# Performance work log

Hardware: AMD Instinct MI355X
Metric: run time of the kernel (lower is better)

Reference implementation:

```python
import jax, jax.numpy as jnp
import numpy as np

B, S, IN, OUT = 4, 2048, 4096, 4096


def setup_inputs() -> dict:
    key = jax.random.key(0)
    kx, kw, kb = jax.random.split(key, 3)
    x = jax.random.randint(kx, (B, S, IN), -127, 128, dtype=jnp.int8)
    weight = jax.random.randint(kw, (OUT, IN), -127, 128, dtype=jnp.int8)
    # original module initializes bias to zeros(int32); use random int32 to exercise the add
    bias = jax.random.randint(kb, (1, OUT), -1000, 1000, dtype=jnp.int32)
    return {"x": x, "weight": weight, "bias": bias}


def reference(x, weight, bias):
    x_shape = x.shape
    x2 = x.reshape(-1, x_shape[-1])  # [tokens, IN], int8
    # dot_general with preferred_element_type=int32 -> int8 inputs, int32 accumulate
    y = jax.lax.dot_general(
        x2, weight,
        dimension_numbers=(((1,), (1,)), ((), ())),
        preferred_element_type=jnp.int32,
    )  # [tokens, OUT] int32
    y = y + bias  # broadcast [1, OUT] int32
    return y.reshape(*x_shape[:-1], -1)
```

## Files before the change

### kernel.cpp

```cpp
#include <hip/hip_runtime.h>
#include <stdint.h>

#define M_TOT 8192
#define N_TOT 4096
#define K_TOT 4096

typedef int v4i  __attribute__((ext_vector_type(4)));
typedef int v16i __attribute__((ext_vector_type(16)));

__device__ __forceinline__ void gload_lds16(const void* g, void* l) {
    __builtin_amdgcn_global_load_lds(
        (const __attribute__((address_space(1))) unsigned int*)g,
        (__attribute__((address_space(3))) unsigned int*)l,
        16, 0, 0);
}

#define WAIT_VMCNT0() __builtin_amdgcn_s_waitcnt(0x0f70)
#define WAIT_VMCNT8() __builtin_amdgcn_s_waitcnt(0x0f78)

__global__ __launch_bounds__(256) void pack_i32_to_i8(
        const int4* __restrict__ src, int* __restrict__ dst, int n4) {
    int idx = blockIdx.x * 1024 + threadIdx.x;
#pragma unroll
    for (int u = 0; u < 4; ++u, idx += 256) {
        const int4 a = src[idx];
        dst[idx] = (a.x & 255) | ((a.y & 255) << 8) |
                   ((a.z & 255) << 16) | (a.w << 24);
    }
}

__global__ __launch_bounds__(256, 1) void i8gemm_bias(
        const signed char* __restrict__ x,
        const signed char* __restrict__ w,
        const int* __restrict__ bias,
        int* __restrict__ out) {
    __shared__ __align__(16) signed char la[3][256 * 64];
    __shared__ __align__(16) signed char lb[3][256 * 64];

    const int tid  = threadIdx.x;
    const int lane = tid & 63;
    const int wv   = tid >> 6;
    const int l31  = lane & 31;
    const int kh   = lane >> 5;
    const int wr   = wv >> 1;
    const int wc   = wv & 1;

    const int flat = blockIdx.y * gridDim.x + blockIdx.x;
    const int swz  = (flat & 7) * 64 + (flat >> 3);
    const int bn0  = (swz & 15) * 256;
    const int bm0  = (swz >> 4) * 256;

    int bv[4];
#pragma unroll
    for (int j = 0; j < 4; ++j) bv[j] = bias[bn0 + wc * 128 + j * 32 + l31];
    v16i acc[4][4];
#pragma unroll
    for (int i = 0; i < 4; ++i)
#pragma unroll
        for (int j = 0; j < 4; ++j)
#pragma unroll
            for (int r = 0; r < 16; ++r) acc[i][j][r] = bv[j];

    const int fc = (lane & 3) ^ ((lane >> 3) & 3);
    const signed char* pa = x + (long)(bm0 + wv * 64 + (lane >> 2)) * K_TOT + fc * 16;
    const signed char* pb = w + (long)(bn0 + wv * 64 + (lane >> 2)) * K_TOT + fc * 16;
    const int lbase = wv * 64 * 64;

    const int swr = (l31 >> 1) & 3;

    signed char* A0 = &la[0][0]; signed char* A1 = &la[1][0]; signed char* A2 = &la[2][0];
    signed char* B0 = &lb[0][0]; signed char* B1 = &lb[1][0]; signed char* B2 = &lb[2][0];

#pragma unroll
    for (int i = 0; i < 4; ++i) {
        gload_lds16(pa + (long)i * 16 * K_TOT, A0 + lbase + i * 1024);
        gload_lds16(pb + (long)i * 16 * K_TOT, B0 + lbase + i * 1024);
    }
#pragma unroll
    for (int i = 0; i < 4; ++i) {
        gload_lds16(pa + 64 + (long)i * 16 * K_TOT, A1 + lbase + i * 1024);
        gload_lds16(pb + 64 + (long)i * 16 * K_TOT, B1 + lbase + i * 1024);
    }

    const int NT = K_TOT / 64;
    for (int kt = 0; kt < NT; ++kt) {
        if (kt == NT - 1) { WAIT_VMCNT0(); } else { WAIT_VMCNT8(); }
        __builtin_amdgcn_s_barrier();
        __builtin_amdgcn_sched_barrier(0);

        if (kt + 2 < NT) {
            const long k0 = (long)(kt + 2) * 64;
#pragma unroll
            for (int i = 0; i < 4; ++i) {
                gload_lds16(pa + k0 + (long)i * 16 * K_TOT, A2 + lbase + i * 1024);
                gload_lds16(pb + k0 + (long)i * 16 * K_TOT, B2 + lbase + i * 1024);
            }
        }
        __builtin_amdgcn_sched_barrier(0);

        v4i af[2][4], bf[2][4];
#pragma unroll
        for (int kk = 0; kk < 2; ++kk) {
            const int cs = ((kk * 2 + kh) ^ swr) * 16;
#pragma unroll
            for (int i = 0; i < 4; ++i) {
                af[kk][i] = *(const v4i*)(A0 + (wr * 128 + i * 32 + l31) * 64 + cs);
                bf[kk][i] = *(const v4i*)(B0 + (wc * 128 + i * 32 + l31) * 64 + cs);
            }
        }
        __builtin_amdgcn_sched_barrier(0);

#pragma unroll
        for (int kk = 0; kk < 2; ++kk)
#pragma unroll
            for (int i = 0; i < 4; ++i)
#pragma unroll
                for (int j = 0; j < 4; ++j)
                    acc[i][j] = __builtin_amdgcn_mfma_i32_32x32x32_i8(
                        af[kk][i], bf[kk][j], acc[i][j], 0, 0, 0);

        signed char* t;
        t = A0; A0 = A1; A1 = A2; A2 = t;
        t = B0; B0 = B1; B1 = B2; B2 = t;
    }

#pragma unroll
    for (int i = 0; i < 4; ++i) {
        const int mbase = bm0 + wr * 128 + i * 32 + 4 * kh;
#pragma unroll
        for (int j = 0; j < 4; ++j) {
            const int n = bn0 + wc * 128 + j * 32 + l31;
#pragma unroll
            for (int r = 0; r < 16; ++r) {
                const int m = mbase + (r & 3) + 8 * (r >> 2);
                out[(long)m * N_TOT + n] = acc[i][j][r];
            }
        }
    }
}

extern "C" void kernel_launch(void* const* d_in, const int* in_sizes, int n_in,
                              void* d_out, int out_size, void* d_ws, size_t ws_size,
                              hipStream_t stream) {
    const int* x32  = (const int*)d_in[0];
    const int* w32  = (const int*)d_in[1];
    const int* bias = (const int*)d_in[2];
    int*       out  = (int*)d_out;

    signed char* xp = (signed char*)d_ws;
    signed char* wp = (signed char*)d_ws + (size_t)M_TOT * K_TOT;

    const int n4x = (M_TOT * K_TOT) / 4;
    const int n4w = (N_TOT * K_TOT) / 4;
    pack_i32_to_i8<<<n4x / 1024, 256, 0, stream>>>((const int4*)x32, (int*)xp, n4x);
    pack_i32_to_i8<<<n4w / 1024, 256, 0, stream>>>((const int4*)w32, (int*)wp, n4w);

    dim3 grid(N_TOT / 256, M_TOT / 256);
    i8gemm_bias<<<grid, 256, 0, stream>>>(xp, wp, bias, out);
}
```

Before: 404.6 us.

## Software-pipeline LDS fragment reads against MFMA across k-halves

Splits each 64-wide k tile into two halves with separate register fragment sets. The first half of the next tile is read from LDS during the current tile's second-half MFMAs, with the wait and barrier moved mid-iteration. This is meant to hide LDS read latency behind matrix-core work instead of stalling before each tile's MFMAs. It needs more registers, and the waitcnt and barrier placement now also waits on LDS counters, which risks correctness if it is wrong.

```diff
diff --git a/kernel.cpp b/kernel.cpp
--- a/kernel.cpp
+++ b/kernel.cpp
@@ -15,8 +15,11 @@
         16, 0, 0);
 }
 
-#define WAIT_VMCNT0() __builtin_amdgcn_s_waitcnt(0x0f70)
-#define WAIT_VMCNT8() __builtin_amdgcn_s_waitcnt(0x0f78)
+#define WAIT_V8_L0() __builtin_amdgcn_s_waitcnt(0x0078)
+#define WAIT_V0_L0() __builtin_amdgcn_s_waitcnt(0x0070)
+#define WAIT_V8()    __builtin_amdgcn_s_waitcnt(0x0f78)
+#define SBAR()       __builtin_amdgcn_s_barrier()
+#define SFENCE()     __builtin_amdgcn_sched_barrier(0)
 
 __global__ __launch_bounds__(256) void pack_i32_to_i8(
         const int4* __restrict__ src, int* __restrict__ dst, int n4) {
@@ -66,7 +69,11 @@
     const signed char* pb = w + (long)(bn0 + wv * 64 + (lane >> 2)) * K_TOT + fc * 16;
     const int lbase = wv * 64 * 64;
 
-    const int swr = (l31 >> 1) & 3;
+    const int swr  = (l31 >> 1) & 3;
+    const int aoff = (wr * 128 + l31) * 64;
+    const int boff = (wc * 128 + l31) * 64;
+    const int cs0  = ((kh    ) ^ swr) * 16;
+    const int cs1  = ((2 + kh) ^ swr) * 16;
 
     signed char* A0 = &la[0][0]; signed char* A1 = &la[1][0]; signed char* A2 = &la[2][0];
     signed char* B0 = &lb[0][0]; signed char* B1 = &lb[1][0]; signed char* B2 = &lb[2][0];
@@ -81,13 +88,26 @@
         gload_lds16(pa + 64 + (long)i * 16 * K_TOT, A1 + lbase + i * 1024);
         gload_lds16(pb + 64 + (long)i * 16 * K_TOT, B1 + lbase + i * 1024);
     }
+    WAIT_V8();
+    SBAR();
+    SFENCE();
+
+    v4i a0[4], b0[4], a1[4], b1[4];
+#pragma unroll
+    for (int i = 0; i < 4; ++i) {
+        a0[i] = *(const v4i*)(A0 + aoff + i * 2048 + cs0);
+        b0[i] = *(const v4i*)(B0 + boff + i * 2048 + cs0);
+    }
 
     const int NT = K_TOT / 64;
     for (int kt = 0; kt < NT; ++kt) {
-        if (kt == NT - 1) { WAIT_VMCNT0(); } else { WAIT_VMCNT8(); }
-        __builtin_amdgcn_s_barrier();
-        __builtin_amdgcn_sched_barrier(0);
-
+        SFENCE();
+#pragma unroll
+        for (int i = 0; i < 4; ++i) {
+            a1[i] = *(const v4i*)(A0 + aoff + i * 2048 + cs1);
+            b1[i] = *(const v4i*)(B0 + boff + i * 2048 + cs1);
+        }
+        SFENCE();
         if (kt + 2 < NT) {
             const long k0 = (long)(kt + 2) * 64;
 #pragma unroll
@@ -96,28 +116,32 @@
                 gload_lds16(pb + k0 + (long)i * 16 * K_TOT, B2 + lbase + i * 1024);
             }
         }
-        __builtin_amdgcn_sched_barrier(0);
-
-        v4i af[2][4], bf[2][4];
+        SFENCE();
 #pragma unroll
-        for (int kk = 0; kk < 2; ++kk) {
-            const int cs = ((kk * 2 + kh) ^ swr) * 16;
+        for (int i = 0; i < 4; ++i)
+#pragma unroll
+            for (int j = 0; j < 4; ++j)
+                acc[i][j] = __builtin_amdgcn_mfma_i32_32x32x32_i8(
+                    a0[i], b0[j], acc[i][j], 0, 0, 0);
+        SFENCE();
+        if (kt + 1 < NT) {
+            if (kt + 2 < NT) { WAIT_V8_L0(); } else { WAIT_V0_L0(); }
+            SFENCE();
+            SBAR();
+            SFENCE();
 #pragma unroll
             for (int i = 0; i < 4; ++i) {
-                af[kk][i] = *(const v4i*)(A0 + (wr * 128 + i * 32 + l31) * 64 + cs);
-                bf[kk][i] = *(const v4i*)(B0 + (wc * 128 + i * 32 + l31) * 64 + cs);
+                a0[i] = *(const v4i*)(A1 + aoff + i * 2048 + cs0);
+                b0[i] = *(const v4i*)(B1 + boff + i * 2048 + cs0);
             }
+            SFENCE();
         }
-        __builtin_amdgcn_sched_barrier(0);
-
 #pragma unroll
-        for (int kk = 0; kk < 2; ++kk)
+        for (int i = 0; i < 4; ++i)
 #pragma unroll
-            for (int i = 0; i < 4; ++i)
-#pragma unroll
-                for (int j = 0; j < 4; ++j)
-                    acc[i][j] = __builtin_amdgcn_mfma_i32_32x32x32_i8(
-                        af[kk][i], bf[kk][j], acc[i][j], 0, 0, 0);
+            for (int j = 0; j < 4; ++j)
+                acc[i][j] = __builtin_amdgcn_mfma_i32_32x32x32_i8(
+                    a1[i], b1[j], acc[i][j], 0, 0, 0);
 
         signed char* t;
         t = A0; A0 = A1; A1 = A2; A2 = t;
```

After: 403.6 us. No clear change (-0.2%).
